# Performance work log

Measured on AMD Instinct MI355X. Metric: run time of the kernel, lower is better.

The kernel has to match this reference:

```python
import jax, jax.numpy as jnp
import numpy as np

HIDDEN = 1024

def setup_inputs() -> dict:
    key = jax.random.key(0)
    ks = jax.random.split(key, 7)
    B, S, H = 4, 2048, HIDDEN
    scale = 1.0 / np.sqrt(H)
    x = jax.random.normal(ks[0], (B, S, H), dtype=jnp.float32)
    Wq = jax.random.normal(ks[1], (H, H), dtype=jnp.float32) * scale
    Wk = jax.random.normal(ks[2], (H, H), dtype=jnp.float32) * scale
    Wv = jax.random.normal(ks[3], (H, H), dtype=jnp.float32) * scale
    bq = jax.random.normal(ks[4], (H,), dtype=jnp.float32) * 0.01
    bk = jax.random.normal(ks[5], (H,), dtype=jnp.float32) * 0.01
    bv = jax.random.normal(ks[6], (H,), dtype=jnp.float32) * 0.01
    return {"x": x, "Wq": Wq, "bq": bq, "Wk": Wk, "bk": bk, "Wv": Wv, "bv": bv}

def reference(x, Wq, bq, Wk, bk, Wv, bv):
    H = x.shape[-1]
    # Linear layers: y = x @ W^T + b (torch convention)
    Q = jnp.einsum('bsh,oh->bso', x, Wq) + bq
    K = jnp.einsum('bsh,oh->bso', x, Wk) + bk
    V = jnp.einsum('bsh,oh->bso', x, Wv) + bv
    # full O(S^2) score matrix, scaled by sqrt(hidden_dim) as in the source
    scores = jnp.einsum('bqh,bkh->bqk', Q, K) / jnp.sqrt(jnp.asarray(H, x.dtype))
    weights = jax.nn.softmax(scores, axis=-1)  # dropout is identity at inference
    out = jnp.einsum('bqk,bkh->bqh', weights, V)
    return out
```

## Files before the change

### kernel.cpp

```cpp
#include <hip/hip_runtime.h>
#include <hip/hip_bf16.h>

typedef __attribute__((ext_vector_type(8))) short bf16x8;
typedef __attribute__((ext_vector_type(4))) float f32x4;
typedef unsigned short u16;
typedef unsigned int u32;


__device__ __forceinline__ u16 f2bf(float f) {
  union { float f; u32 u; } v; v.f = f;
  u32 r = v.u + 0x7FFFu + ((v.u >> 16) & 1u);
  return (u16)(r >> 16);
}

__device__ __forceinline__ void gload_lds16(const u16* g, u16* l) {
  __builtin_amdgcn_global_load_lds(
      (const __attribute__((address_space(1))) u32*)(const void*)g,
      (__attribute__((address_space(3))) u32*)(void*)l, 16, 0, 0);
}


__global__ __launch_bounds__(256) void cvt_bf16(const float* __restrict__ in,
                                                u16* __restrict__ out, int n) {
  int i = (blockIdx.x * 256 + threadIdx.x) * 8;
  if (i >= n) return;
  const float4* p = (const float4*)(in + i);
  float4 a = p[0], b = p[1];
  union { u16 u[8]; uint4 v; } r;
  r.u[0] = f2bf(a.x); r.u[1] = f2bf(a.y); r.u[2] = f2bf(a.z); r.u[3] = f2bf(a.w);
  r.u[4] = f2bf(b.x); r.u[5] = f2bf(b.y); r.u[6] = f2bf(b.z); r.u[7] = f2bf(b.w);
  *(uint4*)(out + i) = r.v;
}


template<int MODE>
__global__ __launch_bounds__(256) void gemm128(const u16* __restrict__ A,
                                               const u16* __restrict__ B,
                                               const float* __restrict__ bias,
                                               void* __restrict__ out0,
                                               void* __restrict__ out1,
                                               void* __restrict__ out2,
                                               float* __restrict__ lsum,
                                               int lda, int ldb, int nkt,
                                               long Abat, long Bbat) {
  __shared__ u16 As[128 * 64];
  __shared__ u16 Bs[128 * 64];
  const int tid = threadIdx.x;
  const int lane = tid & 63, wv = tid >> 6;
  const int lr = lane & 15, lg = lane >> 4;
  const int wm = (wv >> 1) * 64, wn = (wv & 1) * 64;
  const int bm = blockIdx.x * 128, bn = blockIdx.y * 128;
  const int bz = blockIdx.z;
  const u16* Ab = A + (size_t)Abat * bz;
  const u16* Bb = B + (size_t)Bbat * bz;

  f32x4 acc[4][4];
#pragma unroll
  for (int i = 0; i < 4; ++i)
#pragma unroll
    for (int j = 0; j < 4; ++j) acc[i][j] = (f32x4)0.0f;

  for (int kt = 0; kt < nkt; ++kt) {
    const int k0 = kt * 64;
#pragma unroll
    for (int i = 0; i < 4; ++i) {
      int id = i * 256 + tid;
      int row = id >> 3, c = id & 7;
      int cg = c ^ (row & 7);
      gload_lds16(Ab + (size_t)(bm + row) * lda + k0 + cg * 8, As + id * 8);
      gload_lds16(Bb + (size_t)(bn + row) * ldb + k0 + cg * 8, Bs + id * 8);
    }
    __syncthreads();
#pragma unroll
    for (int kk = 0; kk < 2; ++kk) {
      bf16x8 a[4], b[4];
#pragma unroll
      for (int mt = 0; mt < 4; ++mt) {
        int row = wm + mt * 16 + lr;
        int kc = (kk * 4 + lg) ^ (row & 7);
        a[mt] = *(const bf16x8*)(As + row * 64 + kc * 8);
      }
#pragma unroll
      for (int nt = 0; nt < 4; ++nt) {
        int row = wn + nt * 16 + lr;
        int kc = (kk * 4 + lg) ^ (row & 7);
        b[nt] = *(const bf16x8*)(Bs + row * 64 + kc * 8);
      }
#pragma unroll
      for (int mt = 0; mt < 4; ++mt)
#pragma unroll
        for (int nt = 0; nt < 4; ++nt)
          acc[mt][nt] = __builtin_amdgcn_mfma_f32_16x16x32_bf16(a[mt], b[nt], acc[mt][nt], 0, 0, 0);
    }
    __syncthreads();
  }

  if constexpr (MODE == 0) {
    const int sel = bn >> 10;
#pragma unroll
    for (int nt = 0; nt < 4; ++nt) {
      int gcol = bn + wn + nt * 16 + lr;
      int col = gcol & 1023;
      float bv = bias[gcol];
#pragma unroll
      for (int mt = 0; mt < 4; ++mt) {
        int grow0 = bm + wm + mt * 16 + lg * 4;
        if (sel < 2) {
          u16* o = sel ? (u16*)out1 : (u16*)out0;
#pragma unroll
          for (int r = 0; r < 4; ++r)
            o[(size_t)(grow0 + r) * 1024 + col] = f2bf(acc[mt][nt][r] + bv);
        } else {
          u16* o = (u16*)out2;
          int batch = grow0 >> 11, s = grow0 & 2047;
          union { u16 u[4]; uint2 v; } pk;
#pragma unroll
          for (int r = 0; r < 4; ++r) pk.u[r] = f2bf(acc[mt][nt][r] + bv);
          *(uint2*)(o + (((size_t)(batch * 1024 + col)) << 11) + s) = pk.v;
        }
      }
    }
  } else if constexpr (MODE == 2) {
    u16* P = (u16*)out0 + (size_t)2048 * 2048 * bz;
    float psum[4][4];
#pragma unroll
    for (int mt = 0; mt < 4; ++mt)
#pragma unroll
      for (int r = 0; r < 4; ++r) psum[mt][r] = 0.0f;
#pragma unroll
    for (int nt = 0; nt < 4; ++nt) {
      int gcol = bn + wn + nt * 16 + lr;
#pragma unroll
      for (int mt = 0; mt < 4; ++mt) {
        int grow0 = bm + wm + mt * 16 + lg * 4;
#pragma unroll
        for (int r = 0; r < 4; ++r) {
          float e = __expf(acc[mt][nt][r] * 0.03125f);
          P[(size_t)(grow0 + r) * 2048 + gcol] = f2bf(e);
          psum[mt][r] += e;
        }
      }
    }
#pragma unroll
    for (int mt = 0; mt < 4; ++mt)
#pragma unroll
      for (int r = 0; r < 4; ++r) {
#pragma unroll
        for (int off = 1; off < 16; off <<= 1)
          psum[mt][r] += __shfl_xor(psum[mt][r], off);
      }
    if (lr == 0) {
#pragma unroll
      for (int mt = 0; mt < 4; ++mt) {
        int grow0 = bm + wm + mt * 16 + lg * 4;
#pragma unroll
        for (int r = 0; r < 4; ++r)
          atomicAdd(&lsum[bz * 2048 + grow0 + r], psum[mt][r]);
      }
    }
  } else {
    float* o = (float*)out0 + (size_t)2048 * 1024 * bz;
    const float* lrow = lsum + bz * 2048;
    float inv[4][4];
#pragma unroll
    for (int mt = 0; mt < 4; ++mt) {
      int grow0 = bm + wm + mt * 16 + lg * 4;
#pragma unroll
      for (int r = 0; r < 4; ++r) inv[mt][r] = 1.0f / lrow[grow0 + r];
    }
#pragma unroll
    for (int nt = 0; nt < 4; ++nt) {
      int gcol = bn + wn + nt * 16 + lr;
#pragma unroll
      for (int mt = 0; mt < 4; ++mt) {
        int grow0 = bm + wm + mt * 16 + lg * 4;
#pragma unroll
        for (int r = 0; r < 4; ++r)
          o[(size_t)(grow0 + r) * 1024 + gcol] = acc[mt][nt][r] * inv[mt][r];
      }
    }
  }
}


extern "C" void kernel_launch(void* const* d_in, const int* in_sizes, int n_in,
                              void* d_out, int out_size, void* d_ws, size_t ws_size,
                              hipStream_t stream) {
  const float* x  = (const float*)d_in[0];
  const float* Wq = (const float*)d_in[1];
  const float* bq = (const float*)d_in[2];
  const float* Wk = (const float*)d_in[3];
  const float* bk = (const float*)d_in[4];
  const float* Wv = (const float*)d_in[5];
  const float* bv = (const float*)d_in[6];
  float* out = (float*)d_out;

  char* ws = (char*)d_ws;
  u16*   xb   = (u16*)  (ws + ((size_t)0  << 20));
  u16*   wcat = (u16*)  (ws + ((size_t)16 << 20));
  float* bcat = (float*)(ws + ((size_t)22 << 20));
  float* lvec = (float*)(ws + ((size_t)23 << 20));
  u16*   qb   = (u16*)  (ws + ((size_t)24 << 20));
  u16*   kb   = (u16*)  (ws + ((size_t)40 << 20));
  u16*   vtb  = (u16*)  (ws + ((size_t)56 << 20));
  u16*   Pb   = (u16*)  (ws + ((size_t)72 << 20));

  hipMemsetAsync(lvec, 0, 8192 * sizeof(float), stream);
  hipMemcpyAsync(bcat,        bq, 1024 * sizeof(float), hipMemcpyDeviceToDevice, stream);
  hipMemcpyAsync(bcat + 1024, bk, 1024 * sizeof(float), hipMemcpyDeviceToDevice, stream);
  hipMemcpyAsync(bcat + 2048, bv, 1024 * sizeof(float), hipMemcpyDeviceToDevice, stream);

  cvt_bf16<<<dim3(4096), dim3(256), 0, stream>>>(x,  xb, 8388608);
  cvt_bf16<<<dim3(512),  dim3(256), 0, stream>>>(Wq, wcat,           1048576);
  cvt_bf16<<<dim3(512),  dim3(256), 0, stream>>>(Wk, wcat + 1048576, 1048576);
  cvt_bf16<<<dim3(512),  dim3(256), 0, stream>>>(Wv, wcat + 2097152, 1048576);

  gemm128<0><<<dim3(64, 24, 1), dim3(256), 0, stream>>>(
      xb, wcat, bcat, qb, kb, vtb, nullptr, 1024, 1024, 16, 0, 0);

  gemm128<2><<<dim3(16, 16, 4), dim3(256), 0, stream>>>(
      qb, kb, nullptr, Pb, nullptr, nullptr, lvec, 1024, 1024, 16,
      (long)2048 * 1024, (long)2048 * 1024);

  gemm128<3><<<dim3(16, 8, 4), dim3(256), 0, stream>>>(
      Pb, vtb, nullptr, out, nullptr, nullptr, lvec, 2048, 2048, 32,
      (long)2048 * 2048, (long)1024 * 2048);
}
```

Measured before the change: 275.9 us.

## Double-buffer GEMM LDS loads, enlarge tiles to 256x256, fuse conversion kernels

Replaces the 128x128 single-buffered GEMM with a templated 512-thread kernel that prefetches the next K tile into a second LDS buffer while computing on the current one. Tiles grow to 256x256 (128x256 for PV), which raises data reuse per block. The four bf16 conversion kernels become one launch, and the bias copies are dropped by passing the bias pointers directly. The larger tiles use up to 128KB of dynamic LDS and give fewer blocks per GEMM, which risks lower occupancy and poor tail balance on a GPU with many CUs.

```diff
diff --git a/kernel.cpp b/kernel.cpp
--- a/kernel.cpp
+++ b/kernel.cpp
@@ -20,74 +20,108 @@
 }
 
 
-__global__ __launch_bounds__(256) void cvt_bf16(const float* __restrict__ in,
-                                                u16* __restrict__ out, int n) {
-  int i = (blockIdx.x * 256 + threadIdx.x) * 8;
-  if (i >= n) return;
-  const float4* p = (const float4*)(in + i);
+__global__ __launch_bounds__(256) void cvt_all(const float* __restrict__ x,
+                                               const float* __restrict__ wq,
+                                               const float* __restrict__ wk,
+                                               const float* __restrict__ wv,
+                                               u16* __restrict__ xb,
+                                               u16* __restrict__ wcat) {
+  const int bid = blockIdx.x;
+  const float* src; u16* dst; size_t base;
+  if (bid < 4096) { src = x; dst = xb; base = (size_t)bid * 2048; }
+  else {
+    int w = bid - 4096, s = w >> 9;
+    src = (s == 0) ? wq : ((s == 1) ? wk : wv);
+    dst = wcat + (size_t)s * 1048576;
+    base = (size_t)(w & 511) * 2048;
+  }
+  size_t i = base + (size_t)threadIdx.x * 8;
+  const float4* p = (const float4*)(src + i);
   float4 a = p[0], b = p[1];
   union { u16 u[8]; uint4 v; } r;
   r.u[0] = f2bf(a.x); r.u[1] = f2bf(a.y); r.u[2] = f2bf(a.z); r.u[3] = f2bf(a.w);
   r.u[4] = f2bf(b.x); r.u[5] = f2bf(b.y); r.u[6] = f2bf(b.z); r.u[7] = f2bf(b.w);
-  *(uint4*)(out + i) = r.v;
-}
-
-
-template<int MODE>
-__global__ __launch_bounds__(256) void gemm128(const u16* __restrict__ A,
-                                               const u16* __restrict__ B,
-                                               const float* __restrict__ bias,
-                                               void* __restrict__ out0,
-                                               void* __restrict__ out1,
-                                               void* __restrict__ out2,
-                                               float* __restrict__ lsum,
-                                               int lda, int ldb, int nkt,
-                                               long Abat, long Bbat) {
-  __shared__ u16 As[128 * 64];
-  __shared__ u16 Bs[128 * 64];
+  *(uint4*)(dst + i) = r.v;
+}
+
+
+template<int MODE, int BM, int BN>
+__global__ __launch_bounds__(512, 2) void gemm_pipe(
+    const u16* __restrict__ A, const u16* __restrict__ B,
+    const float* __restrict__ b0, const float* __restrict__ b1,
+    const float* __restrict__ b2,
+    void* __restrict__ o0, void* __restrict__ o1, void* __restrict__ o2,
+    float* __restrict__ lsum, int lda, int ldb, int nkt,
+    long Abat, long Bbat) {
+  extern __shared__ u16 lds[];
+  constexpr int NMT = BM / 32;
+  constexpr int ANL = BM / 64;
+  constexpr int BNL = BN / 64;
+  constexpr int ASZ = BM * 64, BSZ = BN * 64;
+
   const int tid = threadIdx.x;
   const int lane = tid & 63, wv = tid >> 6;
   const int lr = lane & 15, lg = lane >> 4;
-  const int wm = (wv >> 1) * 64, wn = (wv & 1) * 64;
-  const int bm = blockIdx.x * 128, bn = blockIdx.y * 128;
+  const int wm = wv >> 2, wn = wv & 3;
+  const int bm = blockIdx.x * BM, bn = blockIdx.y * BN;
   const int bz = blockIdx.z;
-  const u16* Ab = A + (size_t)Abat * bz;
-  const u16* Bb = B + (size_t)Bbat * bz;
-
-  f32x4 acc[4][4];
-#pragma unroll
-  for (int i = 0; i < 4; ++i)
+
+  const u16* Ab; const u16* Bb;
+  if constexpr (MODE == 3) {
+    Ab = A;
+    Bb = B + (size_t)Bbat * (bm >> 11);
+  } else {
+    Ab = A + (size_t)Abat * bz;
+    Bb = B + (size_t)Bbat * bz;
+  }
+
+  f32x4 acc[NMT][4];
+#pragma unroll
+  for (int i = 0; i < NMT; ++i)
 #pragma unroll
     for (int j = 0; j < 4; ++j) acc[i][j] = (f32x4)0.0f;
 
+  auto stage = [&](int kt, int buf) {
+    u16* As = lds + buf * (ASZ + BSZ);
+    u16* Bs = As + ASZ;
+    const int k0 = kt * 64;
+#pragma unroll
+    for (int j = 0; j < ANL; ++j) {
+      int id = j * 512 + tid, row = id >> 3, c = id & 7, cg = c ^ (row & 7);
+      gload_lds16(Ab + (size_t)(bm + row) * lda + k0 + cg * 8, As + id * 8);
+    }
+#pragma unroll
+    for (int j = 0; j < BNL; ++j) {
+      int id = j * 512 + tid, row = id >> 3, c = id & 7, cg = c ^ (row & 7);
+      gload_lds16(Bb + (size_t)(bn + row) * ldb + k0 + cg * 8, Bs + id * 8);
+    }
+  };
+
+  stage(0, 0);
+  __syncthreads();
+
   for (int kt = 0; kt < nkt; ++kt) {
-    const int k0 = kt * 64;
-#pragma unroll
-    for (int i = 0; i < 4; ++i) {
-      int id = i * 256 + tid;
-      int row = id >> 3, c = id & 7;
-      int cg = c ^ (row & 7);
-      gload_lds16(Ab + (size_t)(bm + row) * lda + k0 + cg * 8, As + id * 8);
-      gload_lds16(Bb + (size_t)(bn + row) * ldb + k0 + cg * 8, Bs + id * 8);
-    }
-    __syncthreads();
+    if (kt + 1 < nkt) stage(kt + 1, (kt + 1) & 1);
+    __builtin_amdgcn_sched_barrier(0);
+    const u16* As = lds + (kt & 1) * (ASZ + BSZ);
+    const u16* Bs = As + ASZ;
 #pragma unroll
     for (int kk = 0; kk < 2; ++kk) {
-      bf16x8 a[4], b[4];
-#pragma unroll
-      for (int mt = 0; mt < 4; ++mt) {
-        int row = wm + mt * 16 + lr;
+      bf16x8 a[NMT], b[4];
+#pragma unroll
+      for (int mt = 0; mt < NMT; ++mt) {
+        int row = wm * (BM / 2) + mt * 16 + lr;
         int kc = (kk * 4 + lg) ^ (row & 7);
         a[mt] = *(const bf16x8*)(As + row * 64 + kc * 8);
       }
 #pragma unroll
       for (int nt = 0; nt < 4; ++nt) {
-        int row = wn + nt * 16 + lr;
+        int row = wn * 64 + nt * 16 + lr;
         int kc = (kk * 4 + lg) ^ (row & 7);
         b[nt] = *(const bf16x8*)(Bs + row * 64 + kc * 8);
       }
 #pragma unroll
-      for (int mt = 0; mt < 4; ++mt)
+      for (int mt = 0; mt < NMT; ++mt)
 #pragma unroll
         for (int nt = 0; nt < 4; ++nt)
           acc[mt][nt] = __builtin_amdgcn_mfma_f32_16x16x32_bf16(a[mt], b[nt], acc[mt][nt], 0, 0, 0);
@@ -97,21 +131,22 @@
 
   if constexpr (MODE == 0) {
     const int sel = bn >> 10;
+    const float* bp = (sel == 0) ? b0 : ((sel == 1) ? b1 : b2);
 #pragma unroll
     for (int nt = 0; nt < 4; ++nt) {
-      int gcol = bn + wn + nt * 16 + lr;
+      int gcol = bn + wn * 64 + nt * 16 + lr;
       int col = gcol & 1023;
-      float bv = bias[gcol];
-#pragma unroll
-      for (int mt = 0; mt < 4; ++mt) {
-        int grow0 = bm + wm + mt * 16 + lg * 4;
+      float bv = bp[col];
+#pragma unroll
+      for (int mt = 0; mt < NMT; ++mt) {
+        int grow0 = bm + wm * (BM / 2) + mt * 16 + lg * 4;
         if (sel < 2) {
-          u16* o = sel ? (u16*)out1 : (u16*)out0;
+          u16* o = sel ? (u16*)o1 : (u16*)o0;
 #pragma unroll
           for (int r = 0; r < 4; ++r)
             o[(size_t)(grow0 + r) * 1024 + col] = f2bf(acc[mt][nt][r] + bv);
         } else {
-          u16* o = (u16*)out2;
+          u16* o = (u16*)o2;
           int batch = grow0 >> 11, s = grow0 & 2047;
           union { u16 u[4]; uint2 v; } pk;
 #pragma unroll
@@ -121,18 +156,18 @@
       }
     }
   } else if constexpr (MODE == 2) {
-    u16* P = (u16*)out0 + (size_t)2048 * 2048 * bz;
-    float psum[4][4];
-#pragma unroll
-    for (int mt = 0; mt < 4; ++mt)
+    u16* P = (u16*)o0 + (size_t)2048 * 2048 * bz;
+    float psum[NMT][4];
+#pragma unroll
+    for (int mt = 0; mt < NMT; ++mt)
 #pragma unroll
       for (int r = 0; r < 4; ++r) psum[mt][r] = 0.0f;
 #pragma unroll
     for (int nt = 0; nt < 4; ++nt) {
-      int gcol = bn + wn + nt * 16 + lr;
-#pragma unroll
-      for (int mt = 0; mt < 4; ++mt) {
-        int grow0 = bm + wm + mt * 16 + lg * 4;
+      int gcol = bn + wn * 64 + nt * 16 + lr;
+#pragma unroll
+      for (int mt = 0; mt < NMT; ++mt) {
+        int grow0 = bm + wm * (BM / 2) + mt * 16 + lg * 4;
 #pragma unroll
         for (int r = 0; r < 4; ++r) {
           float e = __expf(acc[mt][nt][r] * 0.03125f);
@@ -142,7 +177,7 @@
       }
     }
 #pragma unroll
-    for (int mt = 0; mt < 4; ++mt)
+    for (int mt = 0; mt < NMT; ++mt)
 #pragma unroll
       for (int r = 0; r < 4; ++r) {
 #pragma unroll
@@ -151,32 +186,27 @@
       }
     if (lr == 0) {
 #pragma unroll
-      for (int mt = 0; mt < 4; ++mt) {
-        int grow0 = bm + wm + mt * 16 + lg * 4;
+      for (int mt = 0; mt < NMT; ++mt) {
+        int grow0 = bm + wm * (BM / 2) + mt * 16 + lg * 4;
 #pragma unroll
         for (int r = 0; r < 4; ++r)
           atomicAdd(&lsum[bz * 2048 + grow0 + r], psum[mt][r]);
       }
     }
   } else {
-    float* o = (float*)out0 + (size_t)2048 * 1024 * bz;
-    const float* lrow = lsum + bz * 2048;
-    float inv[4][4];
-#pragma unroll
-    for (int mt = 0; mt < 4; ++mt) {
-      int grow0 = bm + wm + mt * 16 + lg * 4;
-#pragma unroll
-      for (int r = 0; r < 4; ++r) inv[mt][r] = 1.0f / lrow[grow0 + r];
-    }
-#pragma unroll
-    for (int nt = 0; nt < 4; ++nt) {
-      int gcol = bn + wn + nt * 16 + lr;
-#pragma unroll
-      for (int mt = 0; mt < 4; ++mt) {
-        int grow0 = bm + wm + mt * 16 + lg * 4;
+    float* o = (float*)o0;
+#pragma unroll
+    for (int mt = 0; mt < NMT; ++mt) {
+      int grow0 = bm + wm * (BM / 2) + mt * 16 + lg * 4;
+      float inv[4];
+#pragma unroll
+      for (int r = 0; r < 4; ++r) inv[r] = 1.0f / lsum[grow0 + r];
+#pragma unroll
+      for (int nt = 0; nt < 4; ++nt) {
+        int gcol = bn + wn * 64 + nt * 16 + lr;
 #pragma unroll
         for (int r = 0; r < 4; ++r)
-          o[(size_t)(grow0 + r) * 1024 + gcol] = acc[mt][nt][r] * inv[mt][r];
+          o[(size_t)(grow0 + r) * 1024 + gcol] = acc[mt][nt][r] * inv[r];
       }
     }
   }
@@ -198,31 +228,30 @@
   char* ws = (char*)d_ws;
   u16*   xb   = (u16*)  (ws + ((size_t)0  << 20));
   u16*   wcat = (u16*)  (ws + ((size_t)16 << 20));
-  float* bcat = (float*)(ws + ((size_t)22 << 20));
   float* lvec = (float*)(ws + ((size_t)23 << 20));
   u16*   qb   = (u16*)  (ws + ((size_t)24 << 20));
   u16*   kb   = (u16*)  (ws + ((size_t)40 << 20));
   u16*   vtb  = (u16*)  (ws + ((size_t)56 << 20));
   u16*   Pb   = (u16*)  (ws + ((size_t)72 << 20));
 
+  hipFuncSetAttribute((const void*)&gemm_pipe<0, 256, 256>,
+                      hipFuncAttributeMaxDynamicSharedMemorySize, 131072);
+  hipFuncSetAttribute((const void*)&gemm_pipe<2, 256, 256>,
+                      hipFuncAttributeMaxDynamicSharedMemorySize, 131072);
+  hipFuncSetAttribute((const void*)&gemm_pipe<3, 128, 256>,
+                      hipFuncAttributeMaxDynamicSharedMemorySize, 98304);
+
   hipMemsetAsync(lvec, 0, 8192 * sizeof(float), stream);
-  hipMemcpyAsync(bcat,        bq, 1024 * sizeof(float), hipMemcpyDeviceToDevice, stream);
-  hipMemcpyAsync(bcat + 1024, bk, 1024 * sizeof(float), hipMemcpyDeviceToDevice, stream);
-  hipMemcpyAsync(bcat + 2048, bv, 1024 * sizeof(float), hipMemcpyDeviceToDevice, stream);
-
-  cvt_bf16<<<dim3(4096), dim3(256), 0, stream>>>(x,  xb, 8388608);
-  cvt_bf16<<<dim3(512),  dim3(256), 0, stream>>>(Wq, wcat,           1048576);
-  cvt_bf16<<<dim3(512),  dim3(256), 0, stream>>>(Wk, wcat + 1048576, 1048576);
-  cvt_bf16<<<dim3(512),  dim3(256), 0, stream>>>(Wv, wcat + 2097152, 1048576);
-
-  gemm128<0><<<dim3(64, 24, 1), dim3(256), 0, stream>>>(
-      xb, wcat, bcat, qb, kb, vtb, nullptr, 1024, 1024, 16, 0, 0);
-
-  gemm128<2><<<dim3(16, 16, 4), dim3(256), 0, stream>>>(
-      qb, kb, nullptr, Pb, nullptr, nullptr, lvec, 1024, 1024, 16,
-      (long)2048 * 1024, (long)2048 * 1024);
-
-  gemm128<3><<<dim3(16, 8, 4), dim3(256), 0, stream>>>(
-      Pb, vtb, nullptr, out, nullptr, nullptr, lvec, 2048, 2048, 32,
-      (long)2048 * 2048, (long)1024 * 2048);
-}
+  cvt_all<<<dim3(5632), dim3(256), 0, stream>>>(x, Wq, Wk, Wv, xb, wcat);
+
+  gemm_pipe<0, 256, 256><<<dim3(32, 12, 1), dim3(512), 131072, stream>>>(
+      xb, wcat, bq, bk, bv, qb, kb, vtb, nullptr, 1024, 1024, 16, 0, 0);
+
+  gemm_pipe<2, 256, 256><<<dim3(8, 8, 4), dim3(512), 131072, stream>>>(
+      qb, kb, nullptr, nullptr, nullptr, Pb, nullptr, nullptr, lvec,
+      1024, 1024, 16, (long)2048 * 1024, (long)2048 * 1024);
+
+  gemm_pipe<3, 128, 256><<<dim3(64, 4, 1), dim3(512), 98304, stream>>>(
+      Pb, vtb, nullptr, nullptr, nullptr, out, nullptr, nullptr, lvec,
+      2048, 2048, 32, 0, (long)1024 * 2048);
+}
```

Result: faster. 248.6 us (-9.9%).
